# Performance work log

Measured on AMD Instinct MI355X. Metric: run time of the kernel, lower is better.

The kernel has to match this reference:

```python
import jax, jax.numpy as jnp
import numpy as np

V, E, H, B, T = 32000, 512, 1024, 64, 32  # vocab, emb, hidden, batch, max_length


def setup_inputs() -> dict:
    key = jax.random.key(0)
    ks = jax.random.split(key, 10)
    s = 0.02  # small init scale to keep sigmoids/tanh unsaturated
    return {
        "embedding": jax.random.normal(ks[0], (V, E), jnp.float32) * s,
        "Wx": jax.random.normal(ks[1], (E, 4 * H), jnp.float32) * s,
        "bx": jax.random.normal(ks[2], (4 * H,), jnp.float32) * s,
        "Wh": jax.random.normal(ks[3], (H, 4 * H), jnp.float32) * s,
        "bh": jax.random.normal(ks[4], (4 * H,), jnp.float32) * s,
        "Wout": jax.random.normal(ks[5], (H, V), jnp.float32) * s,
        "bout": jax.random.normal(ks[6], (V,), jnp.float32) * s,
        "h0": jax.random.normal(ks[7], (B, H), jnp.float32),
        "c0": jax.random.normal(ks[8], (B, H), jnp.float32),
        "sos_ids": jax.random.randint(ks[9], (B,), 0, V, jnp.int64)
        if jax.config.jax_enable_x64
        else jax.random.randint(ks[9], (B,), 0, V, jnp.int32),
    }


def reference(embedding, Wx, bx, Wh, bh, Wout, bout, h0, c0, sos_ids):
    """Greedy decode loop: embed prev token, 8-gate LSTM cell, vocab
    projection, top-1 selection feeding the next step. Gate order f,i,g,o
    matches the stacked wfx/wix/wgx/wox (+ *h) Linears of MyLSTMUnit.
    Returns logits for all T steps: [T, B, V]."""

    def step(carry, _):
        tok, h, c = carry
        emb = embedding[tok]  # [B, E] per-step gather
        gates = emb @ Wx + bx + h @ Wh + bh  # [B, 4H] fused 8 gate GEMMs
        f, i, g, o = jnp.split(gates, 4, axis=-1)
        f = jax.nn.sigmoid(f)
        i = jax.nn.sigmoid(i)
        g = jnp.tanh(g)
        o = jax.nn.sigmoid(o)
        c = f * c + i * g
        h = o * jnp.tanh(c)
        logits = h @ Wout + bout  # [B, V]
        nxt = jnp.argmax(logits, axis=-1).astype(tok.dtype)  # greedy top-1
        return (nxt, h, c), logits

    (_, _, _), logits_seq = jax.lax.scan(step, (sos_ids, h0, c0), None, length=T)
    return logits_seq  # [T, B, V]
```

## Files before the change

kernel.cpp:

```cpp
#include <hip/hip_runtime.h>


#define VSZ 32000
#define ESZ 512
#define HSZ 1024
#define BSZ 64
#define TSZ 32
#define G4H 4096

typedef unsigned short u16;
typedef unsigned int u32;
typedef unsigned long long u64;
typedef __attribute__((ext_vector_type(8))) short bf16x8;
typedef __attribute__((ext_vector_type(4))) float f32x4;

__device__ __forceinline__ unsigned ordf(float f) {
  unsigned u = __float_as_uint(f);
  return (u & 0x80000000u) ? ~u : (u | 0x80000000u);
}
__device__ __forceinline__ u16 f2bf(float f) {
  u32 u = __float_as_uint(f);
  return (u16)((u + 0x7FFFu + ((u >> 16) & 1u)) >> 16);
}
__device__ __forceinline__ float bf2f(u16 s) {
  return __uint_as_float(((u32)s) << 16);
}
__device__ __forceinline__ void split3(double v, u16& s0, u16& s1, u16& s2) {
  s0 = f2bf((float)v);
  double r = v - (double)bf2f(s0);
  s1 = f2bf((float)r);
  double r2 = r - (double)bf2f(s1);
  s2 = f2bf((float)r2);
}

__device__ __forceinline__ void pack_h(int j, int b, double h,
                                       u16* __restrict__ HA2,
                                       u16* __restrict__ HA3) {
  u16 s0, s1, s2;
  split3(h, s0, s1, s2);
  int kc = j >> 5, kj = j & 31;
  int lane = (b & 15) | ((kj >> 3) << 4);
  int Mt = b >> 4;
  int e = kj & 7;
  HA2[(size_t)(kc * 4 + Mt) * 512 + lane * 8 + e] = s0;
  size_t b3 = ((size_t)(kc * 4 + Mt) * 3) * 512 + lane * 8 + e;
  HA3[b3] = s0;
  HA3[b3 + 512] = s1;
  HA3[b3 + 1024] = s2;
}

__device__ __forceinline__ void pack_e(int k, int b, double v,
                                       u16* __restrict__ EA3) {
  u16 s0, s1, s2;
  split3(v, s0, s1, s2);
  int kc = k >> 5, kj = k & 31;
  int lane = (b & 15) | ((kj >> 3) << 4);
  int Mt = b >> 4;
  int e = kj & 7;
  size_t b3 = ((size_t)(kc * 4 + Mt) * 3) * 512 + lane * 8 + e;
  EA3[b3] = s0;
  EA3[b3 + 512] = s1;
  EA3[b3 + 1024] = s2;
}

__device__ __forceinline__ void ins4(u64 v, u64& t0, u64& t1, u64& t2,
                                     u64& t3) {
  bool g0 = v > t0, g1 = v > t1, g2 = v > t2, g3 = v > t3;
  t3 = g2 ? t2 : (g3 ? v : t3);
  t2 = g1 ? t1 : (g2 ? v : t2);
  t1 = g0 ? t0 : (g1 ? v : t1);
  t0 = g0 ? v : t0;
}
__device__ __forceinline__ void merge4(u64& a0, u64& a1, u64& a2, u64& a3,
                                       u64 b0, u64 b1, u64 b2, u64 b3) {
  u64 m0 = a0 > b3 ? a0 : b3;
  u64 m1 = a1 > b2 ? a1 : b2;
  u64 m2 = a2 > b1 ? a2 : b1;
  u64 m3 = a3 > b0 ? a3 : b0;
  u64 e0 = m0 > m2 ? m0 : m2, e2 = m0 > m2 ? m2 : m0;
  u64 e1 = m1 > m3 ? m1 : m3, e3 = m1 > m3 ? m3 : m1;
  a0 = e0 > e1 ? e0 : e1;
  a1 = e0 > e1 ? e1 : e0;
  a2 = e2 > e3 ? e2 : e3;
  a3 = e2 > e3 ? e3 : e2;
}

__global__ __launch_bounds__(256) void k_init(
    const float* __restrict__ h0, const float* __restrict__ c0,
    const int* __restrict__ sos, const float* __restrict__ emb,
    double* __restrict__ cT64, double* __restrict__ h64,
    u16* __restrict__ HA2, u16* __restrict__ HA3b, u16* __restrict__ EA3) {
  int idx = blockIdx.x * 256 + threadIdx.x;
  int j = idx >> 6, b = idx & 63;
  double h = (double)h0[b * HSZ + j];
  cT64[idx] = (double)c0[b * HSZ + j];
  h64[idx] = h;
  pack_h(j, b, h, HA2, HA3b);
  if (j < ESZ) pack_e(j, b, (double)emb[(size_t)sos[b] * ESZ + j], EA3);
}

__global__ __launch_bounds__(256) void k_wpackL(const float* __restrict__ Wout,
                                                u16* __restrict__ WBL) {
  __shared__ float ls[32][64];
  int tid = threadIdx.x;
  int j0 = blockIdx.x * 64;
  int Nt0 = blockIdx.x * 4;
  for (int kc = 0; kc < 32; ++kc) {
    __syncthreads();
    #pragma unroll
    for (int rr = 0; rr < 8; ++rr) {
      int row = rr * 4 + (tid >> 6);
      ls[row][tid & 63] = Wout[(size_t)(kc * 32 + row) * VSZ + j0 + (tid & 63)];
    }
    __syncthreads();
    int lane = tid & 63, Ntl = tid >> 6;
    int col = Ntl * 16 + (lane & 15);
    int kb = (lane >> 4) * 8;
    alignas(16) u16 hibuf[8];
    #pragma unroll
    for (int e = 0; e < 8; ++e) hibuf[e] = f2bf(ls[kb + e][col]);
    size_t base = ((size_t)((Nt0 + Ntl) * 32 + kc)) * 512 + lane * 8;
    *(bf16x8*)&WBL[base] = *(const bf16x8*)hibuf;
  }
}

__global__ __launch_bounds__(256) void k_wpackG(const float* __restrict__ Wx,
                                                const float* __restrict__ Wh,
                                                u16* __restrict__ WBG) {
  int tid = threadIdx.x;
  int Nt = blockIdx.x;
  int lane = tid & 63, w = tid >> 6;
  int col = Nt * 16 + (lane & 15);
  for (int i = 0; i < 12; ++i) {
    int kc = w * 12 + i;
    int kb = kc * 32 + (lane >> 4) * 8;
    alignas(16) u16 b0[8], b1[8], b2[8];
    #pragma unroll
    for (int e = 0; e < 8; ++e) {
      int k = kb + e;
      float v = (k < ESZ) ? Wx[(size_t)k * G4H + col]
                          : Wh[(size_t)(k - ESZ) * G4H + col];
      u16 s0, s1, s2;
      split3((double)v, s0, s1, s2);
      b0[e] = s0; b1[e] = s1; b2[e] = s2;
    }
    size_t base = ((size_t)(Nt * 48 + kc) * 3) * 512 + lane * 8;
    *(bf16x8*)&WBG[base] = *(const bf16x8*)b0;
    *(bf16x8*)&WBG[base + 512] = *(const bf16x8*)b1;
    *(bf16x8*)&WBG[base + 1024] = *(const bf16x8*)b2;
  }
}

__global__ __launch_bounds__(512) void k_gatescell(
    const u16* __restrict__ EA3, const u16* __restrict__ HA3r,
    const u16* __restrict__ WBG, const float* __restrict__ bx,
    const float* __restrict__ bh, double* __restrict__ cT64,
    double* __restrict__ h64, u16* __restrict__ HA2,
    u16* __restrict__ HA3w) {
  __shared__ double gvL[8][256];
  int tid = threadIdx.x, lane = tid & 63, w = tid >> 6;
  int g = w & 3, kh = w >> 2;
  int q = blockIdx.x;
  int jt = (q & 7) + 8 * ((q >> 3) >> 2);
  int mg = (q >> 3) & 3;
  int Nt = g * 64 + jt;

  double big[4];
  #pragma unroll
  for (int r = 0; r < 4; ++r) big[r] = 0.0;
  f32x4 accs = {0.f, 0.f, 0.f, 0.f};
  const f32x4 zz = {0.f, 0.f, 0.f, 0.f};

  for (int i = 0; i < 24; ++i) {
    int kc = kh * 24 + i;
    const u16* wb = WBG + ((size_t)(Nt * 48 + kc) * 3) * 512 + lane * 8;
    bf16x8 b0 = *(const bf16x8*)wb;
    bf16x8 b1 = *(const bf16x8*)(wb + 512);
    bf16x8 b2 = *(const bf16x8*)(wb + 1024);
    const u16* ha = (kc < 16)
        ? (EA3 + ((size_t)(kc * 4 + mg) * 3) * 512 + lane * 8)
        : (HA3r + ((size_t)((kc - 16) * 4 + mg) * 3) * 512 + lane * 8);
    bf16x8 a0 = *(const bf16x8*)ha;
    bf16x8 a1 = *(const bf16x8*)(ha + 512);
    bf16x8 a2 = *(const bf16x8*)(ha + 1024);
    f32x4 tb = __builtin_amdgcn_mfma_f32_16x16x32_bf16(a0, b0, zz, 0, 0, 0);
    #pragma unroll
    for (int r = 0; r < 4; ++r) big[r] += (double)tb[r];
    accs = __builtin_amdgcn_mfma_f32_16x16x32_bf16(a1, b0, accs, 0, 0, 0);
    accs = __builtin_amdgcn_mfma_f32_16x16x32_bf16(a0, b1, accs, 0, 0, 0);
    accs = __builtin_amdgcn_mfma_f32_16x16x32_bf16(a1, b1, accs, 0, 0, 0);
    accs = __builtin_amdgcn_mfma_f32_16x16x32_bf16(a2, b0, accs, 0, 0, 0);
    accs = __builtin_amdgcn_mfma_f32_16x16x32_bf16(a0, b2, accs, 0, 0, 0);
  }
  #pragma unroll
  for (int r = 0; r < 4; ++r) {
    int bl = (lane >> 4) * 4 + r;
    gvL[w][(lane & 15) * 16 + bl] = big[r] + (double)accs[r];
  }
  __syncthreads();

  if (tid < 256) {
    int jl = tid >> 4, bl = tid & 15;
    int j = jt * 16 + jl, b = mg * 16 + bl;
    double gv0 = (gvL[0][tid] + gvL[4][tid]) + (double)bx[j] + (double)bh[j];
    double gv1 = (gvL[1][tid] + gvL[5][tid]) + (double)bx[1024 + j] +
                 (double)bh[1024 + j];
    double gv2 = (gvL[2][tid] + gvL[6][tid]) + (double)bx[2048 + j] +
                 (double)bh[2048 + j];
    double gv3 = (gvL[3][tid] + gvL[7][tid]) + (double)bx[3072 + j] +
                 (double)bh[3072 + j];
    double c = cT64[(size_t)j * 64 + b];
    double f = 1.0 / (1.0 + exp(-gv0));
    double i = 1.0 / (1.0 + exp(-gv1));
    double gg = tanh(gv2);
    double o = 1.0 / (1.0 + exp(-gv3));
    c = f * c + i * gg;
    double h = o * tanh(c);
    cT64[(size_t)j * 64 + b] = c;
    h64[(size_t)j * 64 + b] = h;
    pack_h(j, b, h, HA2, HA3w);
  }
}

__global__ __launch_bounds__(512) void k_logits_mfma(
    int t, const u16* __restrict__ HA2, const u16* __restrict__ WBL,
    const float* __restrict__ bout, float* __restrict__ out,
    u64* __restrict__ p2) {
  __shared__ f32x4 pacc[4][64][4];
  __shared__ float lv[4][64][17];
  int tid = threadIdx.x, lane = tid & 63, w = tid >> 6;
  int nl = w & 3, half = w >> 2;
  int Nt = blockIdx.x * 4 + nl;
  int colw = Nt * 16 + (lane & 15);
  const u16* wb = WBL + (size_t)Nt * 16384 + lane * 8;
  f32x4 acc[4] = {};

  int kc0 = half * 16;
  #pragma unroll 2
  for (int kk = 0; kk < 16; ++kk) {
    int kc = kc0 + kk;
    bf16x8 bhv = *(const bf16x8*)(wb + (size_t)kc * 512);
    const u16* ha = HA2 + (size_t)kc * 2048 + lane * 8;
    #pragma unroll
    for (int Mt = 0; Mt < 4; ++Mt) {
      bf16x8 ah = *(const bf16x8*)(ha + Mt * 512);
      acc[Mt] = __builtin_amdgcn_mfma_f32_16x16x32_bf16(ah, bhv, acc[Mt], 0, 0, 0);
    }
  }
  if (half == 1) {
    #pragma unroll
    for (int Mt = 0; Mt < 4; ++Mt) pacc[nl][lane][Mt] = acc[Mt];
  }
  __syncthreads();
  if (half == 0) {
    #pragma unroll
    for (int Mt = 0; Mt < 4; ++Mt) acc[Mt] = acc[Mt] + pacc[nl][lane][Mt];
    float bo = bout[colw];
    float* orow = out + (size_t)t * BSZ * VSZ;
    #pragma unroll
    for (int Mt = 0; Mt < 4; ++Mt) {
      #pragma unroll
      for (int r = 0; r < 4; ++r) {
        int row = Mt * 16 + (lane >> 4) * 4 + r;
        float v = acc[Mt][r] + bo;
        orow[(size_t)row * VSZ + colw] = v;
        lv[nl][row][lane & 15] = v;
      }
    }
  }
  __syncthreads();
  if (half == 0) {
    const float* rowp = lv[nl][lane];
    float m1 = rowp[0];
    int i1 = 0;
    float m2 = -__builtin_inff();
    int i2 = 1;
    #pragma unroll
    for (int c = 1; c < 16; ++c) {
      float v = rowp[c];
      bool top = v > m1;
      bool sec = v > m2;
      m2 = top ? m1 : (sec ? v : m2);
      i2 = top ? i1 : (sec ? c : i2);
      m1 = top ? v : m1;
      i1 = top ? c : i1;
    }
    int c1 = Nt * 16 + i1, c2 = Nt * 16 + i2;
    u64 k1 = ((u64)ordf(m1) << 32) | (unsigned)(~c1);
    u64 k2 = ((u64)ordf(m2) << 32) | (unsigned)(~c2);
    size_t slot = (size_t)lane * 2000 + blockIdx.x * 4 + nl;
    p2[slot * 2] = k1;
    p2[slot * 2 + 1] = k2;
  }
}

__global__ __launch_bounds__(256) void k_refine(
    const u64* __restrict__ p2, const double* __restrict__ h64,
    const float* __restrict__ Wout, const float* __restrict__ bout,
    int* __restrict__ tokbuf, const float* __restrict__ emb,
    u16* __restrict__ EA3) {
  __shared__ u64 sm[256][4];
  __shared__ double rr[256][4];
  __shared__ int s_i[4];
  __shared__ int s_sel;
  int b = blockIdx.x, tid = threadIdx.x;
  u64 t0 = 0, t1 = 0, t2 = 0, t3 = 0;
  for (int i = tid; i < 2000; i += 256) {
    u64 x = p2[((size_t)b * 2000 + i) * 2];
    u64 y = p2[((size_t)b * 2000 + i) * 2 + 1];
    ins4(x, t0, t1, t2, t3);
    ins4(y, t0, t1, t2, t3);
  }
  sm[tid][0] = t0; sm[tid][1] = t1; sm[tid][2] = t2; sm[tid][3] = t3;
  __syncthreads();
  for (int off = 128; off > 0; off >>= 1) {
    if (tid < off) {
      u64 a0 = sm[tid][0], a1 = sm[tid][1], a2 = sm[tid][2], a3 = sm[tid][3];
      merge4(a0, a1, a2, a3, sm[tid + off][0], sm[tid + off][1],
             sm[tid + off][2], sm[tid + off][3]);
      sm[tid][0] = a0; sm[tid][1] = a1; sm[tid][2] = a2; sm[tid][3] = a3;
    }
    __syncthreads();
  }
  if (tid < 4) s_i[tid] = (int)(~(u32)(sm[0][tid] & 0xFFFFFFFFull));
  __syncthreads();
  int i0 = s_i[0], i1 = s_i[1], i2 = s_i[2], i3 = s_i[3];
  double a0 = 0.0, a1 = 0.0, a2 = 0.0, a3 = 0.0;
  #pragma unroll
  for (int q = 0; q < 4; ++q) {
    int k = tid * 4 + q;
    double h = h64[(size_t)k * 64 + b];
    const float* wr = Wout + (size_t)k * VSZ;
    a0 += h * (double)wr[i0];
    a1 += h * (double)wr[i1];
    a2 += h * (double)wr[i2];
    a3 += h * (double)wr[i3];
  }
  rr[tid][0] = a0; rr[tid][1] = a1; rr[tid][2] = a2; rr[tid][3] = a3;
  __syncthreads();
  for (int off = 128; off > 0; off >>= 1) {
    if (tid < off) {
      rr[tid][0] += rr[tid + off][0];
      rr[tid][1] += rr[tid + off][1];
      rr[tid][2] += rr[tid + off][2];
      rr[tid][3] += rr[tid + off][3];
    }
    __syncthreads();
  }
  if (tid == 0) {
    double v0 = rr[0][0] + (double)bout[i0];
    double v1 = rr[0][1] + (double)bout[i1];
    double v2 = rr[0][2] + (double)bout[i2];
    double v3 = rr[0][3] + (double)bout[i3];
    double bv = v0; int bi = i0;
    if (v1 > bv || (v1 == bv && i1 < bi)) { bv = v1; bi = i1; }
    if (v2 > bv || (v2 == bv && i2 < bi)) { bv = v2; bi = i2; }
    if (v3 > bv || (v3 == bv && i3 < bi)) { bv = v3; bi = i3; }
    tokbuf[b] = bi;
    s_sel = bi;
  }
  __syncthreads();
  int tokf = s_sel;
  int k = tid * 2;
  pack_e(k, b, (double)emb[(size_t)tokf * ESZ + k], EA3);
  pack_e(k + 1, b, (double)emb[(size_t)tokf * ESZ + k + 1], EA3);
}


__global__ __launch_bounds__(256) void k_initF(const float* __restrict__ h0,
                                               const float* __restrict__ c0,
                                               float* __restrict__ hT,
                                               float* __restrict__ cT) {
  int idx = blockIdx.x * 256 + threadIdx.x;
  int j = idx >> 6, b = idx & 63;
  hT[idx] = h0[b * HSZ + j];
  cT[idx] = c0[b * HSZ + j];
}

__global__ __launch_bounds__(256) void k_gatesF(
    int t, const int* __restrict__ sos, const u64* __restrict__ partials,
    const float* __restrict__ emb, const float* __restrict__ Wx,
    const float* __restrict__ Wh, const float* __restrict__ hT,
    float* __restrict__ gP) {
  __shared__ float xs[128 * 64];
  __shared__ u64 s_red[256];
  __shared__ int s_tok[64];
  int tid = threadIdx.x;
  if (t == 0) {
    if (tid < 64) s_tok[tid] = sos[tid];
  } else {
    int b = tid >> 2, q = tid & 3;
    u64 best = 0ull;
    int i0 = q * 63, i1 = i0 + 63;
    if (i1 > 250) i1 = 250;
    for (int i = i0; i < i1; ++i) {
      u64 v = partials[b * 512 + i];
      if (v > best) best = v;
    }
    s_red[tid] = best;
    __syncthreads();
    if (q == 0) {
      u64 m = best;
      #pragma unroll
      for (int k = 1; k < 4; ++k) {
        u64 v = s_red[tid + k];
        if (v > m) m = v;
      }
      s_tok[b] = (int)(~(unsigned)(m & 0xFFFFFFFFull));
    }
  }
  __syncthreads();
  int colblk = blockIdx.x & 63, ks = blockIdx.x >> 6;
  int col = colblk * 16 + (tid & 15);
  int b0 = (tid >> 4) * 4;
  float acc[4][4];
  #pragma unroll
  for (int g = 0; g < 4; ++g)
    #pragma unroll
    for (int bb = 0; bb < 4; ++bb) acc[g][bb] = 0.f;
  for (int kc = 0; kc < 3; ++kc) {
    int k0 = ks * 384 + kc * 128;
    __syncthreads();
    if (k0 < 512) {
      int b = tid & 63;
      int kk0 = (tid >> 6) * 32;
      const float* erow = emb + (size_t)s_tok[b] * ESZ + k0 + kk0;
      #pragma unroll
      for (int i = 0; i < 32; i += 4) {
        float4 v = *(const float4*)(erow + i);
        xs[(kk0 + i) * 64 + b] = v.x;
        xs[(kk0 + i + 1) * 64 + b] = v.y;
        xs[(kk0 + i + 2) * 64 + b] = v.z;
        xs[(kk0 + i + 3) * 64 + b] = v.w;
      }
    } else {
      const float* src = hT + (size_t)(k0 - 512) * 64;
      #pragma unroll
      for (int i = 0; i < 8192; i += 1024)
        *(float4*)&xs[i + tid * 4] = *(const float4*)(src + i + tid * 4);
    }
    __syncthreads();
    const float* Wb = (k0 < 512) ? (Wx + (size_t)k0 * G4H + col)
                                 : (Wh + (size_t)(k0 - 512) * G4H + col);
    #pragma unroll 4
    for (int kk = 0; kk < 128; ++kk) {
      float4 xv = *(const float4*)&xs[kk * 64 + b0];
      const float* wr = Wb + (size_t)kk * G4H;
      float w0 = wr[0], w1 = wr[1024], w2 = wr[2048], w3 = wr[3072];
      acc[0][0] += w0 * xv.x; acc[0][1] += w0 * xv.y;
      acc[0][2] += w0 * xv.z; acc[0][3] += w0 * xv.w;
      acc[1][0] += w1 * xv.x; acc[1][1] += w1 * xv.y;
      acc[1][2] += w1 * xv.z; acc[1][3] += w1 * xv.w;
      acc[2][0] += w2 * xv.x; acc[2][1] += w2 * xv.y;
      acc[2][2] += w2 * xv.z; acc[2][3] += w2 * xv.w;
      acc[3][0] += w3 * xv.x; acc[3][1] += w3 * xv.y;
      acc[3][2] += w3 * xv.z; acc[3][3] += w3 * xv.w;
    }
  }
  #pragma unroll
  for (int g = 0; g < 4; ++g) {
    float4 v = make_float4(acc[g][0], acc[g][1], acc[g][2], acc[g][3]);
    *(float4*)&gP[((size_t)ks * G4H + g * 1024 + col) * 64 + b0] = v;
  }
}

__global__ __launch_bounds__(256) void k_cellF(const float* __restrict__ gP,
                                               const float* __restrict__ bx,
                                               const float* __restrict__ bh,
                                               float* __restrict__ hT,
                                               float* __restrict__ cT) {
  int flat = (blockIdx.x * 256 + threadIdx.x) * 2;
  int j = flat >> 6;
  float2 gv[4];
  #pragma unroll
  for (int g = 0; g < 4; ++g) {
    size_t base = ((size_t)g * 1024 + j) * 64 + (flat & 63);
    float2 s = *(const float2*)&gP[base];
    #pragma unroll
    for (int ks = 1; ks < 4; ++ks) {
      float2 p = *(const float2*)&gP[(size_t)ks * 262144 + base];
      s.x += p.x; s.y += p.y;
    }
    float bias = bx[g * 1024 + j] + bh[g * 1024 + j];
    s.x += bias; s.y += bias;
    gv[g] = s;
  }
  float2 c = *(const float2*)&cT[flat];
  float fx = 1.f / (1.f + expf(-gv[0].x)), fy = 1.f / (1.f + expf(-gv[0].y));
  float ix = 1.f / (1.f + expf(-gv[1].x)), iy = 1.f / (1.f + expf(-gv[1].y));
  float gx = tanhf(gv[2].x), gy = tanhf(gv[2].y);
  float ox = 1.f / (1.f + expf(-gv[3].x)), oy = 1.f / (1.f + expf(-gv[3].y));
  float cx = fx * c.x + ix * gx, cy = fy * c.y + iy * gy;
  float hx = ox * tanhf(cx), hy = oy * tanhf(cy);
  *(float2*)&cT[flat] = make_float2(cx, cy);
  *(float2*)&hT[flat] = make_float2(hx, hy);
}

__global__ __launch_bounds__(512) void k_logitsF(
    int t, const float* __restrict__ hT, const float* __restrict__ Wout,
    const float* __restrict__ bout, float* __restrict__ out,
    u64* __restrict__ partials) {
  __shared__ float hs[128 * 64];
  int tid = threadIdx.x;
  int lane = tid & 63;
  int bg = tid >> 6;
  int b0 = bg * 8;
  int j0 = blockIdx.x * 128 + lane * 2;
  float a0[8], a1[8];
  #pragma unroll
  for (int i = 0; i < 8; ++i) { a0[i] = 0.f; a1[i] = 0.f; }
  for (int kc = 0; kc < 8; ++kc) {
    int k0 = kc * 128;
    __syncthreads();
    #pragma unroll
    for (int i = 0; i < 8192; i += 2048)
      *(float4*)&hs[i + tid * 4] =
          *(const float4*)&hT[(size_t)k0 * 64 + i + tid * 4];
    __syncthreads();
    #pragma unroll 4
    for (int kk = 0; kk < 128; ++kk) {
      float2 wv = *(const float2*)(Wout + (size_t)(k0 + kk) * VSZ + j0);
      const float* hrow = &hs[kk * 64 + b0];
      float4 h0v = *(const float4*)(hrow);
      float4 h1v = *(const float4*)(hrow + 4);
      a0[0] += h0v.x * wv.x; a1[0] += h0v.x * wv.y;
      a0[1] += h0v.y * wv.x; a1[1] += h0v.y * wv.y;
      a0[2] += h0v.z * wv.x; a1[2] += h0v.z * wv.y;
      a0[3] += h0v.w * wv.x; a1[3] += h0v.w * wv.y;
      a0[4] += h1v.x * wv.x; a1[4] += h1v.x * wv.y;
      a0[5] += h1v.y * wv.x; a1[5] += h1v.y * wv.y;
      a0[6] += h1v.z * wv.x; a1[6] += h1v.z * wv.y;
      a0[7] += h1v.w * wv.x; a1[7] += h1v.w * wv.y;
    }
  }
  float bo0 = bout[j0], bo1 = bout[j0 + 1];
  float* orow = out + (size_t)t * BSZ * VSZ;
  #pragma unroll
  for (int bb = 0; bb < 8; ++bb) {
    float v0 = a0[bb] + bo0, v1 = a1[bb] + bo1;
    *(float2*)(orow + (size_t)(b0 + bb) * VSZ + j0) = make_float2(v0, v1);
    float m; int mi;
    if (v1 > v0) { m = v1; mi = j0 + 1; } else { m = v0; mi = j0; }
    u64 key = ((u64)ordf(m) << 32) | (unsigned)(~mi);
    #pragma unroll
    for (int s = 32; s > 0; s >>= 1) {
      u64 o = __shfl_xor(key, s, 64);
      if (o > key) key = o;
    }
    if (lane == bb) partials[(size_t)(b0 + bb) * 512 + blockIdx.x] = key;
  }
}

extern "C" void kernel_launch(void* const* d_in, const int* in_sizes, int n_in,
                              void* d_out, int out_size, void* d_ws,
                              size_t ws_size, hipStream_t stream) {
  const float* emb  = (const float*)d_in[0];
  const float* Wx   = (const float*)d_in[1];
  const float* bx   = (const float*)d_in[2];
  const float* Wh   = (const float*)d_in[3];
  const float* bh   = (const float*)d_in[4];
  const float* Wout = (const float*)d_in[5];
  const float* bout = (const float*)d_in[6];
  const float* h0   = (const float*)d_in[7];
  const float* c0   = (const float*)d_in[8];
  const int*   sos  = (const int*)d_in[9];
  float* out = (float*)d_out;

  bool mfma = ws_size >= 123814912ULL;

  char* base = (char*)d_ws;
  double* cT64 = (double*)(base);
  double* h64  = (double*)(base + 524288);
  u16*    HA2  = (u16*)(base + 1048576);
  u16*    HA3a = (u16*)(base + 1179648);
  u16*    HA3b = (u16*)(base + 1572864);
  u16*    EA3  = (u16*)(base + 1966080);
  int*    tokb = (int*)(base + 2162688);
  u64*    p2   = (u64*)(base + 2166784);
  u16*    WBL  = (u16*)(base + 4214784);
  u16*    WBG  = (u16*)(base + 69750784);
  float* hT = (float*)(base);
  float* cT = (float*)(base + 262144);
  float* gP = (float*)(base + 524288);
  u64* partials = (u64*)(base + 4718592);

  if (mfma) {
    k_wpackL<<<500, 256, 0, stream>>>(Wout, WBL);
    k_wpackG<<<256, 256, 0, stream>>>(Wx, Wh, WBG);
    k_init<<<256, 256, 0, stream>>>(h0, c0, sos, emb, cT64, h64, HA2, HA3b,
                                    EA3);
    for (int t = 0; t < TSZ; ++t) {
      const u16* HA3r = (t & 1) ? HA3a : HA3b;
      u16* HA3w = (t & 1) ? HA3b : HA3a;
      k_gatescell<<<256, 512, 0, stream>>>(EA3, HA3r, WBG, bx, bh, cT64, h64,
                                           HA2, HA3w);
      k_logits_mfma<<<500, 512, 0, stream>>>(t, HA2, WBL, bout, out, p2);
      if (t + 1 < TSZ)
        k_refine<<<64, 256, 0, stream>>>(p2, h64, Wout, bout, tokb, emb, EA3);
    }
  } else {
    k_initF<<<256, 256, 0, stream>>>(h0, c0, hT, cT);
    for (int t = 0; t < TSZ; ++t) {
      k_gatesF<<<256, 256, 0, stream>>>(t, sos, partials, emb, Wx, Wh, hT, gP);
      k_cellF<<<128, 256, 0, stream>>>(gP, bx, bh, hT, cT);
      k_logitsF<<<250, 512, 0, stream>>>(t, hT, Wout, bout, out, partials);
    }
  }
}
```

Measured before the change: 1.514 ms.

## Coalesce logits stores via LDS and pre-reduce top-4 candidates per block

The logits kernel now stages results in shared memory and writes each row segment with float4 stores from all 512 threads, replacing scattered 4-byte column-strided stores. The per-tile top-2 candidates are also merged within the block into a top-4 list, so the refine kernel scans 500 entries per batch row instead of 2000 pairs. The k-loop unroll goes from 2 to 4. This adds extra block barriers and a serial merge done by one wave, and the block-level pruning assumes that keeping the top-4 per block is enough for the later refinement step.

```diff
diff --git a/kernel.cpp b/kernel.cpp
--- a/kernel.cpp
+++ b/kernel.cpp
@@ -228,6 +228,7 @@
     u64* __restrict__ p2) {
   __shared__ f32x4 pacc[4][64][4];
   __shared__ float lv[4][64][17];
+  __shared__ u64 kk[4][64][2];
   int tid = threadIdx.x, lane = tid & 63, w = tid >> 6;
   int nl = w & 3, half = w >> 2;
   int Nt = blockIdx.x * 4 + nl;
@@ -236,9 +237,9 @@
   f32x4 acc[4] = {};
 
   int kc0 = half * 16;
-  #pragma unroll 2
-  for (int kk = 0; kk < 16; ++kk) {
-    int kc = kc0 + kk;
+  #pragma unroll 4
+  for (int kq = 0; kq < 16; ++kq) {
+    int kc = kc0 + kq;
     bf16x8 bhv = *(const bf16x8*)(wb + (size_t)kc * 512);
     const u16* ha = HA2 + (size_t)kc * 2048 + lane * 8;
     #pragma unroll
@@ -256,19 +257,27 @@
     #pragma unroll
     for (int Mt = 0; Mt < 4; ++Mt) acc[Mt] = acc[Mt] + pacc[nl][lane][Mt];
     float bo = bout[colw];
-    float* orow = out + (size_t)t * BSZ * VSZ;
     #pragma unroll
     for (int Mt = 0; Mt < 4; ++Mt) {
       #pragma unroll
       for (int r = 0; r < 4; ++r) {
         int row = Mt * 16 + (lane >> 4) * 4 + r;
-        float v = acc[Mt][r] + bo;
-        orow[(size_t)row * VSZ + colw] = v;
-        lv[nl][row][lane & 15] = v;
+        lv[nl][row][lane & 15] = acc[Mt][r] + bo;
       }
     }
   }
   __syncthreads();
+  {
+    float* orow = out + (size_t)t * BSZ * VSZ;
+    int r = tid >> 3, cc0 = (tid & 7) * 8;
+    int nl2 = cc0 >> 4, c2 = cc0 & 15;
+    float tmp[8];
+    #pragma unroll
+    for (int u = 0; u < 8; ++u) tmp[u] = lv[nl2][r][c2 + u];
+    float* dst = orow + (size_t)r * VSZ + blockIdx.x * 64 + cc0;
+    *(float4*)dst = make_float4(tmp[0], tmp[1], tmp[2], tmp[3]);
+    *(float4*)(dst + 4) = make_float4(tmp[4], tmp[5], tmp[6], tmp[7]);
+  }
   if (half == 0) {
     const float* rowp = lv[nl][lane];
     float m1 = rowp[0];
@@ -286,11 +295,22 @@
       i1 = top ? c : i1;
     }
     int c1 = Nt * 16 + i1, c2 = Nt * 16 + i2;
-    u64 k1 = ((u64)ordf(m1) << 32) | (unsigned)(~c1);
-    u64 k2 = ((u64)ordf(m2) << 32) | (unsigned)(~c2);
-    size_t slot = (size_t)lane * 2000 + blockIdx.x * 4 + nl;
-    p2[slot * 2] = k1;
-    p2[slot * 2 + 1] = k2;
+    kk[nl][lane][0] = ((u64)ordf(m1) << 32) | (unsigned)(~c1);
+    kk[nl][lane][1] = ((u64)ordf(m2) << 32) | (unsigned)(~c2);
+  }
+  __syncthreads();
+  if (half == 0 && nl == 0) {
+    u64 t0 = 0, t1 = 0, t2 = 0, t3 = 0;
+    #pragma unroll
+    for (int q = 0; q < 4; ++q) {
+      ins4(kk[q][lane][0], t0, t1, t2, t3);
+      ins4(kk[q][lane][1], t0, t1, t2, t3);
+    }
+    size_t s4 = ((size_t)lane * 500 + blockIdx.x) * 4;
+    p2[s4] = t0;
+    p2[s4 + 1] = t1;
+    p2[s4 + 2] = t2;
+    p2[s4 + 3] = t3;
   }
 }
 
@@ -305,11 +325,12 @@
   __shared__ int s_sel;
   int b = blockIdx.x, tid = threadIdx.x;
   u64 t0 = 0, t1 = 0, t2 = 0, t3 = 0;
-  for (int i = tid; i < 2000; i += 256) {
-    u64 x = p2[((size_t)b * 2000 + i) * 2];
-    u64 y = p2[((size_t)b * 2000 + i) * 2 + 1];
-    ins4(x, t0, t1, t2, t3);
-    ins4(y, t0, t1, t2, t3);
+  for (int i = tid; i < 500; i += 256) {
+    const u64* pp = &p2[((size_t)b * 500 + i) * 4];
+    ins4(pp[0], t0, t1, t2, t3);
+    ins4(pp[1], t0, t1, t2, t3);
+    ins4(pp[2], t0, t1, t2, t3);
+    ins4(pp[3], t0, t1, t2, t3);
   }
   sm[tid][0] = t0; sm[tid][1] = t1; sm[tid][2] = t2; sm[tid][3] = t3;
   __syncthreads();
```

After: 1.458 ms. 1.04x faster.
